# Optimization experiments

Measured on AMD Instinct MI355X. Metric: run time of the kernel, lower is better.

Reference implementation:

```python
import jax, jax.numpy as jnp
import numpy as np

N = 8192
E = 524288
IN_DIM = 128
HID = 256
OUT_DIM = 128
N_LAYERS = 3
N_HEADS = 4
HEAD_DIM = HID // N_HEADS


def setup_inputs() -> dict:
    key = jax.random.key(0)
    ks = jax.random.split(key, 12)
    s = 0.05
    return {
        "x": jax.random.normal(ks[0], (N, IN_DIM), dtype=jnp.float32),
        "edge_index": jax.random.randint(ks[1], (2, E), 0, N, dtype=jnp.int64),
        "W_in": jax.random.normal(ks[2], (HID, IN_DIM), dtype=jnp.float32) * s,
        "b_in": jnp.zeros((HID,), dtype=jnp.float32),
        "plasticity": jnp.ones((N_LAYERS,), dtype=jnp.float32),
        "synaptic": jnp.ones((N_LAYERS,), dtype=jnp.float32),
        "in_proj_w": jax.random.normal(ks[3], (3 * HID, HID), dtype=jnp.float32) * s,
        "in_proj_b": jnp.zeros((3 * HID,), dtype=jnp.float32),
        "out_proj_w": jax.random.normal(ks[4], (HID, HID), dtype=jnp.float32) * s,
        "out_proj_b": jnp.zeros((HID,), dtype=jnp.float32),
        "W_out": jax.random.normal(ks[5], (OUT_DIM, HID), dtype=jnp.float32) * s,
        "b_out": jnp.zeros((OUT_DIM,), dtype=jnp.float32),
    }


def _forward(x, edge_index, W_in, b_in, plasticity, synaptic,
             in_proj_w, in_proj_b, out_proj_w, out_proj_b, W_out, b_out):
    src, dst = edge_index[0], edge_index[1]  # x_j = x[src], aggregate at dst (source_to_target)
    x = x @ W_in.T + b_in  # [N, HID]
    for i in range(N_LAYERS):
        x = x * jax.nn.sigmoid(plasticity[i])
        # message: x_j * sigmoid(synaptic) (scalar edge weight); aggr='add'
        agg = jax.ops.segment_sum(x[src], dst, num_segments=N)  # gather-scatter-add
        x = jax.nn.leaky_relu(agg * jax.nn.sigmoid(synaptic[i]), negative_slope=0.01)
    # MultiheadAttention over all N nodes (seq_len=N, batch=1)
    qkv = x @ in_proj_w.T + in_proj_b  # [N, 3*HID]
    q, k, v = jnp.split(qkv, 3, axis=-1)
    q = q.reshape(N, N_HEADS, HEAD_DIM).transpose(1, 0, 2)  # [h, n, d]
    k = k.reshape(N, N_HEADS, HEAD_DIM).transpose(1, 0, 2)
    v = v.reshape(N, N_HEADS, HEAD_DIM).transpose(1, 0, 2)
    scores = jnp.einsum("hnd,hmd->hnm", q, k) / np.sqrt(HEAD_DIM).astype(np.float32)
    attn = jax.nn.softmax(scores, axis=-1)
    o = jnp.einsum("hnm,hmd->hnd", attn, v)  # [h, n, d]
    o = o.transpose(1, 0, 2).reshape(N, HID)
    x = o @ out_proj_w.T + out_proj_b
    return x @ W_out.T + b_out  # [N, OUT_DIM]


def reference(x, edge_index, W_in, b_in, plasticity, synaptic,
              in_proj_w, in_proj_b, out_proj_w, out_proj_b, W_out, b_out):
    return _forward(x, edge_index, W_in, b_in, plasticity, synaptic,
                    in_proj_w, in_proj_b, out_proj_w, out_proj_b, W_out, b_out)
```

## Files before the change

### kernel.cpp

```cpp
#include <hip/hip_runtime.h>
#include <hip/hip_bf16.h>
#include <float.h>

#define N_NODES 8192
#define NEDGE   524288
#define IND     128
#define HID     256
#define OUTD    128
#define NHEAD   4
#define HD      64

typedef short short8 __attribute__((ext_vector_type(8)));
typedef short short4v __attribute__((ext_vector_type(4)));
typedef float f32x4  __attribute__((ext_vector_type(4)));
typedef float f32x16 __attribute__((ext_vector_type(16)));
typedef unsigned int u32x4 __attribute__((ext_vector_type(4)));

__device__ __forceinline__ float sigmoidf_(float x) { return 1.0f / (1.0f + expf(-x)); }

__device__ __forceinline__ unsigned short f2bf(float f) {
    __hip_bfloat16 b = __float2bfloat16(f);
    return __builtin_bit_cast(unsigned short, b);
}
__device__ __forceinline__ float bf2f(unsigned short u) {
    __hip_bfloat16 b = __builtin_bit_cast(__hip_bfloat16, u);
    return __bfloat162float(b);
}
__device__ __forceinline__ void split3(float x, unsigned short& a, unsigned short& b, unsigned short& c) {
    a = f2bf(x); float r = x - bf2f(a);
    b = f2bf(r); r = r - bf2f(b);
    c = f2bf(r);
}
__device__ __forceinline__ void split2(float x, unsigned short& a, unsigned short& b) {
    a = f2bf(x); float r = x - bf2f(a);
    b = f2bf(r);
}
__device__ __forceinline__ unsigned int cvtpk(float lo, float hi) {
    unsigned int r;
    asm("v_cvt_pk_bf16_f32 %0, %1, %2" : "=v"(r) : "v"(lo), "v"(hi));
    return r;
}
__device__ __forceinline__ void plswap(unsigned int& a, unsigned int& b) {
    asm volatile("v_permlane32_swap_b32 %0, %1" : "+v"(a), "+v"(b));
}
__device__ __forceinline__ void gll16(const void* g, void* l) {
    __builtin_amdgcn_global_load_lds(
        (const __attribute__((address_space(1))) void*)g,
        (__attribute__((address_space(3))) void*)l, 16, 0, 0);
}
__device__ __forceinline__ f32x16 mfma32(short8 a, short8 b, f32x16 c) {
    return __builtin_amdgcn_mfma_f32_32x32x16_bf16(a, b, c, 0, 0, 0);
}

__global__ void hist_kernel(const int* __restrict__ ei, int* __restrict__ deg)
{
    int e = blockIdx.x * blockDim.x + threadIdx.x;
    if (e < NEDGE) atomicAdd(&deg[ei[NEDGE + e]], 1);
}

__global__ __launch_bounds__(1024) void scan_kernel(
    const int* __restrict__ deg, int* __restrict__ row_ptr, int* __restrict__ cursor)
{
    __shared__ int sh[1024];
    const int t = threadIdx.x;
    int v[8]; int s = 0;
    #pragma unroll
    for (int i = 0; i < 8; ++i) { v[i] = deg[t * 8 + i]; s += v[i]; }
    sh[t] = s; __syncthreads();
    for (int off = 1; off < 1024; off <<= 1) {
        int add = (t >= off) ? sh[t - off] : 0;
        __syncthreads();
        sh[t] += add;
        __syncthreads();
    }
    int base = sh[t] - s;
    #pragma unroll
    for (int i = 0; i < 8; ++i) {
        row_ptr[t * 8 + i] = base;
        cursor[t * 8 + i]  = base;
        base += v[i];
    }
    if (t == 1023) row_ptr[N_NODES] = base;
}

__global__ void scatter_kernel(const int* __restrict__ ei, int* __restrict__ cursor,
                               int* __restrict__ esrc)
{
    int e = blockIdx.x * blockDim.x + threadIdx.x;
    if (e < NEDGE) {
        int d = ei[NEDGE + e];
        int p = atomicAdd(&cursor[d], 1);
        esrc[p] = ei[e];
    }
}

__global__ __launch_bounds__(256) void split_w_kernel(
    const float* __restrict__ w, unsigned short* __restrict__ Wc, int elems)
{
    const int i = (blockIdx.x * 256 + threadIdx.x) * 8;
    if (i >= elems) return;
    float4 a = *(const float4*)(w + i);
    float4 b = *(const float4*)(w + i + 4);
    float v[8] = {a.x, a.y, a.z, a.w, b.x, b.y, b.z, b.w};
    short8 c0, c1, c2;
    #pragma unroll
    for (int j = 0; j < 8; ++j) {
        unsigned short p, q, r;
        split3(v[j], p, q, r);
        c0[j] = (short)p; c1[j] = (short)q; c2[j] = (short)r;
    }
    *(short8*)(Wc + i) = c0;
    *(short8*)(Wc + elems + i) = c1;
    *(short8*)(Wc + 2 * elems + i) = c2;
}

__global__ __launch_bounds__(256) void aggregate_sliced_kernel(
    const float* __restrict__ hin, float* __restrict__ hout,
    const int* __restrict__ row_ptr, const int* __restrict__ esrc,
    const float* __restrict__ plas, const float* __restrict__ syn, int layer)
{
    const int b = blockIdx.x;
    const int xs = b & 7, g = b >> 3;
    const int slice = xs & 3, halfn = xs >> 2;
    const int t = threadIdx.x;
    const int dst = halfn * 4096 + g * 4 + (t >> 6);
    const int col = slice * 64 + (t & 63);
    const int st = row_ptr[dst], en = row_ptr[dst + 1];
    float a0 = 0.f, a1 = 0.f, a2 = 0.f, a3 = 0.f;
    int e = st;
    for (; e + 4 <= en; e += 4) {
        int s0 = esrc[e], s1 = esrc[e + 1], s2 = esrc[e + 2], s3 = esrc[e + 3];
        a0 += hin[(size_t)s0 * HID + col];
        a1 += hin[(size_t)s1 * HID + col];
        a2 += hin[(size_t)s2 * HID + col];
        a3 += hin[(size_t)s3 * HID + col];
    }
    float acc = (a0 + a1) + (a2 + a3);
    for (; e < en; ++e) acc += hin[(size_t)esrc[e] * HID + col];
    const float scale = sigmoidf_(plas[layer]) * sigmoidf_(syn[layer]);
    float x = acc * scale;
    hout[(size_t)dst * HID + col] = (x > 0.f) ? x : 0.01f * x;
}

__global__ __launch_bounds__(256) void aggregate_sliced_split_kernel(
    const float* __restrict__ hin,
    unsigned short* __restrict__ H0, unsigned short* __restrict__ H1,
    unsigned short* __restrict__ H2,
    const int* __restrict__ row_ptr, const int* __restrict__ esrc,
    const float* __restrict__ plas, const float* __restrict__ syn, int layer)
{
    const int b = blockIdx.x;
    const int xs = b & 7, g = b >> 3;
    const int slice = xs & 3, halfn = xs >> 2;
    const int t = threadIdx.x;
    const int dst = halfn * 4096 + g * 4 + (t >> 6);
    const int col = slice * 64 + (t & 63);
    const int st = row_ptr[dst], en = row_ptr[dst + 1];
    float a0 = 0.f, a1 = 0.f, a2 = 0.f, a3 = 0.f;
    int e = st;
    for (; e + 4 <= en; e += 4) {
        int s0 = esrc[e], s1 = esrc[e + 1], s2 = esrc[e + 2], s3 = esrc[e + 3];
        a0 += hin[(size_t)s0 * HID + col];
        a1 += hin[(size_t)s1 * HID + col];
        a2 += hin[(size_t)s2 * HID + col];
        a3 += hin[(size_t)s3 * HID + col];
    }
    float acc = (a0 + a1) + (a2 + a3);
    for (; e < en; ++e) acc += hin[(size_t)esrc[e] * HID + col];
    const float scale = sigmoidf_(plas[layer]) * sigmoidf_(syn[layer]);
    float x = acc * scale;
    x = (x > 0.f) ? x : 0.01f * x;
    unsigned short p, q, r;
    split3(x, p, q, r);
    H0[(size_t)dst * HID + col] = p;
    H1[(size_t)dst * HID + col] = q;
    H2[(size_t)dst * HID + col] = r;
}

template<int NT, int NA, bool SOUT>
__global__ __launch_bounds__(256) void mfma_gemm_kernel(
    const unsigned short* __restrict__ A0, const unsigned short* __restrict__ A1,
    const unsigned short* __restrict__ A2,
    const unsigned short* __restrict__ Wc, const float* __restrict__ bias,
    float* __restrict__ Cf, unsigned short* __restrict__ C0, unsigned short* __restrict__ C1,
    int M, int Nn, int K)
{
    const int t = threadIdx.x;
    const int wv = t >> 6, lane = t & 63;
    const int l31 = lane & 31, l5 = lane >> 5;
    const int wm = wv & 1, wn = wv >> 1;
    const int m0 = blockIdx.x * 64 + wm * 32;
    const int n0 = blockIdx.y * 64 + wn * 32;
    const int mrow = m0 + l31;
    const int nrow = n0 + l31;
    const size_t NK = (size_t)Nn * K;

    f32x16 o;
    #pragma unroll
    for (int r = 0; r < 16; ++r) o[r] = 0.f;

    for (int k = 0; k < K; k += 16) {
        const int kk = k + l5 * 8;
        short8 af[NA];
        af[0] = *(const short8*)(A0 + (size_t)mrow * K + kk);
        af[1] = *(const short8*)(A1 + (size_t)mrow * K + kk);
        if (NA > 2) af[2] = *(const short8*)(A2 + (size_t)mrow * K + kk);
        const unsigned short* wp = Wc + (size_t)nrow * K + kk;
        short8 w0 = *(const short8*)(wp);
        short8 w1 = *(const short8*)(wp + NK);
        if (NT == 6) {
            short8 w2 = *(const short8*)(wp + 2 * NK);
            o = mfma32(w0, af[2], o);
            o = mfma32(w1, af[1], o);
            o = mfma32(w2, af[0], o);
            o = mfma32(w0, af[1], o);
            o = mfma32(w1, af[0], o);
            o = mfma32(w0, af[0], o);
        } else {
            o = mfma32(w0, af[1], o);
            o = mfma32(w1, af[0], o);
            o = mfma32(w0, af[0], o);
        }
    }

    #pragma unroll
    for (int g = 0; g < 4; ++g) {
        const int nb = n0 + g * 8 + l5 * 4;
        const float4 b4 = *(const float4*)(bias + nb);
        float v0 = o[4 * g + 0] + b4.x;
        float v1 = o[4 * g + 1] + b4.y;
        float v2 = o[4 * g + 2] + b4.z;
        float v3 = o[4 * g + 3] + b4.w;
        if (!SOUT) {
            float4 st = {v0, v1, v2, v3};
            *(float4*)(Cf + (size_t)mrow * Nn + nb) = st;
        } else {
            unsigned short h0, h1, p0, p1, q0, q1, r0, r1;
            split2(v0, h0, h1); split2(v1, p0, p1);
            split2(v2, q0, q1); split2(v3, r0, r1);
            short4v s0 = {(short)h0, (short)p0, (short)q0, (short)r0};
            short4v s1 = {(short)h1, (short)p1, (short)q1, (short)r1};
            *(short4v*)(C0 + (size_t)mrow * Nn + nb) = s0;
            *(short4v*)(C1 + (size_t)mrow * Nn + nb) = s1;
        }
    }
}

__global__ __launch_bounds__(256) void split_kernel(
    const float* __restrict__ qkv,
    unsigned short* __restrict__ Kc0, unsigned short* __restrict__ Kc1,
    unsigned short* __restrict__ Kc2, unsigned short* __restrict__ Vt0)
{
    __shared__ unsigned short vts[64 * 80];
    const int h  = blockIdx.y;
    const int n0 = blockIdx.x * 64;
    const int t  = threadIdx.x;
    const int r  = t >> 2;
    const int n  = n0 + r;
    const int dc = (t & 3) * 16;

    {
        const float* kp = qkv + (size_t)n * 768 + 256 + h * 64 + dc;
        float kv[16];
        #pragma unroll
        for (int i = 0; i < 16; i += 4) {
            float4 f = *(const float4*)(kp + i);
            kv[i] = f.x; kv[i+1] = f.y; kv[i+2] = f.z; kv[i+3] = f.w;
        }
        #pragma unroll
        for (int half = 0; half < 2; ++half) {
            short8 c0, c1, c2;
            #pragma unroll
            for (int j = 0; j < 8; ++j) {
                unsigned short a, b, c;
                split3(kv[half * 8 + j], a, b, c);
                c0[j] = (short)a; c1[j] = (short)b; c2[j] = (short)c;
            }
            const int pos = ((dc >> 3) + half) ^ (n & 7);
            const size_t base = ((size_t)(h * 8192 + n)) * 64 + pos * 8;
            *(short8*)(Kc0 + base) = c0;
            *(short8*)(Kc1 + base) = c1;
            *(short8*)(Kc2 + base) = c2;
        }
    }
    {
        const float* vp = qkv + (size_t)n * 768 + 512 + h * 64 + dc;
        #pragma unroll
        for (int i = 0; i < 16; i += 4) {
            float4 f = *(const float4*)(vp + i);
            float vv[4] = {f.x, f.y, f.z, f.w};
            #pragma unroll
            for (int k2 = 0; k2 < 4; ++k2)
                vts[(dc + i + k2) * 80 + r] = f2bf(vv[k2]);
        }
    }
    __syncthreads();
    #pragma unroll
    for (int i = 0; i < 2; ++i) {
        const int q = t * 2 + i;
        const int d = q >> 3, nc = q & 7;
        const int g = nc >> 2, c = nc & 3;
        short8 vv = *(const short8*)(&vts[d * 80 + nc * 8]);
        const size_t dst = ((size_t)(h * 64 + d)) * 8192 + n0 + g * 32 + ((c ^ (d & 3)) * 8);
        *(short8*)(Vt0 + dst) = vv;
    }
}

__global__ __launch_bounds__(256, 4) void attn_mfma_kernel(
    const float* __restrict__ qkv,
    const unsigned short* __restrict__ Kc0, const unsigned short* __restrict__ Kc1,
    const unsigned short* __restrict__ Kc2, const unsigned short* __restrict__ Vt0,
    unsigned short* __restrict__ Op16, float* __restrict__ Ml)
{
    __shared__ __align__(16) char smem[32768];
    const int h    = blockIdx.y;
    const int quar = blockIdx.z;
    const int n0   = blockIdx.x * 128;
    const int t    = threadIdx.x;
    const int wv   = t >> 6;
    const int lane = t & 63;
    const int l31  = lane & 31, l5 = lane >> 5;
    const int qbase = n0 + wv * 32;

    const float QSC = 0.125f * 1.4426950408889634f;
    short8 qf[3][4];
    #pragma unroll
    for (int ks = 0; ks < 4; ++ks) {
        const float* qp = qkv + (size_t)(qbase + l31) * 768 + h * 64 + ks * 16 + l5 * 8;
        float4 qa = *(const float4*)qp, qb4 = *(const float4*)(qp + 4);
        float qv[8] = {qa.x, qa.y, qa.z, qa.w, qb4.x, qb4.y, qb4.z, qb4.w};
        #pragma unroll
        for (int j = 0; j < 8; ++j) {
            unsigned short a, b, c;
            split3(qv[j] * QSC, a, b, c);
            qf[0][ks][j] = (short)a;
            qf[1][ks][j] = (short)b;
            qf[2][ks][j] = (short)c;
        }
    }

    int koff[4], voff[2][2];
    #pragma unroll
    for (int ks = 0; ks < 4; ++ks)
        koff[ks] = l31 * 128 + (((ks * 2 + l5) ^ (l31 & 7)) * 16);
    #pragma unroll
    for (int ks = 0; ks < 2; ++ks)
        #pragma unroll
        for (int db = 0; db < 2; ++db) {
            const int d = db * 32 + l31;
            voff[ks][db] = 12288 + d * 64 + (((ks * 2 + l5) ^ (d & 3)) * 16);
        }

    const char* sgb[4];
    int ldso[4];
    #pragma unroll
    for (int i = 0; i < 4; ++i) {
        const int s = wv * 4 + i;
        if (s < 12) {
            const int c = s >> 2, rb = s & 3;
            const unsigned short* base = (c == 0) ? Kc0 : (c == 1) ? Kc1 : Kc2;
            const int row = rb * 8 + (lane >> 3);
            sgb[i] = (const char*)(base + ((size_t)(h * 8192 + quar * 2048 + row)) * 64 + (lane & 7) * 8);
            ldso[i] = c * 4096 + rb * 1024;
        } else {
            const int v = s - 12;
            const int d = v * 16 + (lane >> 2);
            sgb[i] = (const char*)(Vt0 + ((size_t)(h * 64 + d)) * 8192 + quar * 2048 + (lane & 3) * 8);
            ldso[i] = 12288 + v * 1024;
        }
    }
    const size_t ktstride = (wv < 3) ? 4096 : 64;

    auto STAGE = [&](int kt, int bb) {
        #pragma unroll
        for (int i = 0; i < 4; ++i)
            gll16(sgb[i] + (size_t)kt * ktstride, &smem[bb * 16384 + ldso[i]]);
    };

    f32x16 o[2];
    #pragma unroll
    for (int db = 0; db < 2; ++db)
        #pragma unroll
        for (int r = 0; r < 16; ++r) o[db][r] = 0.f;
    float mr = -FLT_MAX, ls = 0.f;

    STAGE(0, 0);
    __syncthreads();

    for (int kt = 0; kt < 64; ++kt) {
        const int bb = kt & 1;
        if (kt < 63) STAGE(kt + 1, bb ^ 1);
        const char* buf = &smem[bb * 16384];

        f32x16 s;
        #pragma unroll
        for (int r = 0; r < 16; ++r) s[r] = 0.f;

        __builtin_amdgcn_s_setprio(1);
        #pragma unroll
        for (int ks = 0; ks < 4; ++ks) {
            const int off = koff[ks];
            short8 k0 = *(const short8*)(buf + off);
            short8 k1 = *(const short8*)(buf + 4096 + off);
            short8 k2 = *(const short8*)(buf + 8192 + off);
            s = mfma32(k0, qf[2][ks], s);
            s = mfma32(k1, qf[1][ks], s);
            s = mfma32(k2, qf[0][ks], s);
            s = mfma32(k0, qf[1][ks], s);
            s = mfma32(k1, qf[0][ks], s);
            s = mfma32(k0, qf[0][ks], s);
        }
        __builtin_amdgcn_s_setprio(0);

        float mx = s[0];
        #pragma unroll
        for (int r = 1; r < 16; ++r) mx = fmaxf(mx, s[r]);
        mx = fmaxf(mx, __shfl_xor(mx, 32));
        if (__any(mx > mr + 12.0f)) {
            const float mn = fmaxf(mr, mx);
            const float alpha = exp2f(mr - mn);
            mr = mn;
            ls *= alpha;
            o[0] *= alpha;
            o[1] *= alpha;
        }
        float ps = 0.f;
        #pragma unroll
        for (int r = 0; r < 16; ++r) {
            float p = exp2f(s[r] - mr);
            s[r] = p;
            ps += p;
        }
        ps += __shfl_xor(ps, 32);
        ls += ps;

        short8 pb[2];
        #pragma unroll
        for (int ks = 0; ks < 2; ++ks) {
            const int rb = ks * 8;
            unsigned int A0 = cvtpk(s[rb + 0], s[rb + 1]);
            unsigned int A1 = cvtpk(s[rb + 2], s[rb + 3]);
            unsigned int B0 = cvtpk(s[rb + 4], s[rb + 5]);
            unsigned int B1 = cvtpk(s[rb + 6], s[rb + 7]);
            plswap(A0, B0);
            plswap(A1, B1);
            u32x4 pw; pw[0] = A0; pw[1] = A1; pw[2] = B0; pw[3] = B1;
            pb[ks] = __builtin_bit_cast(short8, pw);
        }

        __builtin_amdgcn_s_setprio(1);
        #pragma unroll
        for (int ks = 0; ks < 2; ++ks) {
            #pragma unroll
            for (int db = 0; db < 2; ++db) {
                short8 v = *(const short8*)(buf + voff[ks][db]);
                o[db] = mfma32(v, pb[ks], o[db]);
            }
        }
        __builtin_amdgcn_s_setprio(0);

        __syncthreads();
    }

    {
        const int q = qbase + l31;
        unsigned short* opq = Op16 + ((size_t)((quar * 4 + h) * 8192 + q)) * 64;
        #pragma unroll
        for (int db = 0; db < 2; ++db) {
            #pragma unroll
            for (int tq = 0; tq < 4; ++tq) {
                const int d0 = db * 32 + tq * 8 + l5 * 4;
                unsigned int w0 = cvtpk(o[db][4 * tq + 0], o[db][4 * tq + 1]);
                unsigned int w1 = cvtpk(o[db][4 * tq + 2], o[db][4 * tq + 3]);
                uint2 st = {w0, w1};
                *(uint2*)(opq + d0) = st;
            }
        }
        if (l5 == 0) {
            Ml[((size_t)(quar * 4 + h) * 2 + 0) * 8192 + q] = mr;
            Ml[((size_t)(quar * 4 + h) * 2 + 1) * 8192 + q] = ls;
        }
    }
}

__global__ __launch_bounds__(256) void combine_kernel(
    const unsigned short* __restrict__ Op16, const float* __restrict__ Ml,
    unsigned short* __restrict__ aO0, unsigned short* __restrict__ aO1)
{
    const int idx = blockIdx.x * 256 + threadIdx.x;
    const int c = idx & 3;
    const int q = (idx >> 2) & 8191;
    const int h = idx >> 15;
    float m[4], l[4];
    float mg = -FLT_MAX;
    #pragma unroll
    for (int s = 0; s < 4; ++s) {
        m[s] = Ml[((size_t)(s * 4 + h) * 2 + 0) * 8192 + q];
        l[s] = Ml[((size_t)(s * 4 + h) * 2 + 1) * 8192 + q];
        mg = fmaxf(mg, m[s]);
    }
    float w[4], denom = 0.f;
    #pragma unroll
    for (int s = 0; s < 4; ++s) {
        w[s] = exp2f(m[s] - mg);
        denom += l[s] * w[s];
    }
    const float inv = 1.f / denom;
    float acc[16] = {};
    #pragma unroll
    for (int s = 0; s < 4; ++s) {
        const unsigned short* p = Op16 + ((size_t)(s * 4 + h) * 8192 + q) * 64 + c * 16;
        short8 v0 = *(const short8*)(p);
        short8 v1 = *(const short8*)(p + 8);
        #pragma unroll
        for (int i = 0; i < 8; ++i) {
            acc[i]     += w[s] * bf2f((unsigned short)v0[i]);
            acc[i + 8] += w[s] * bf2f((unsigned short)v1[i]);
        }
    }
    unsigned short* d0 = aO0 + (size_t)q * 256 + h * 64 + c * 16;
    unsigned short* d1 = aO1 + (size_t)q * 256 + h * 64 + c * 16;
    short8 o0, o1;
    #pragma unroll
    for (int i = 0; i < 8; ++i) {
        unsigned short a, b;
        split2(acc[i] * inv, a, b);
        o0[i] = (short)a; o1[i] = (short)b;
    }
    *(short8*)(d0) = o0;
    *(short8*)(d1) = o1;
    #pragma unroll
    for (int i = 0; i < 8; ++i) {
        unsigned short a, b;
        split2(acc[i + 8] * inv, a, b);
        o0[i] = (short)a; o1[i] = (short)b;
    }
    *(short8*)(d0 + 8) = o0;
    *(short8*)(d1 + 8) = o1;
}

extern "C" void kernel_launch(void* const* d_in, const int* in_sizes, int n_in,
                              void* d_out, int out_size, void* d_ws, size_t ws_size,
                              hipStream_t stream)
{
    const float* x     = (const float*)d_in[0];
    const int*   ei    = (const int*)  d_in[1];
    const float* W_in  = (const float*)d_in[2];
    const float* b_in  = (const float*)d_in[3];
    const float* plas  = (const float*)d_in[4];
    const float* syn   = (const float*)d_in[5];
    const float* inpw  = (const float*)d_in[6];
    const float* inpb  = (const float*)d_in[7];
    const float* outpw = (const float*)d_in[8];
    const float* outpb = (const float*)d_in[9];
    const float* Wout  = (const float*)d_in[10];
    const float* bout  = (const float*)d_in[11];
    float* out = (float*)d_out;

    char* ws = (char*)d_ws;
    float* h    = (float*)(ws + 0);
    float* h2   = (float*)(ws + (8u  << 20));
    float* qkv  = (float*)(ws + (16u << 20));
    unsigned short* xc0  = (unsigned short*)(ws + (16u << 20));
    unsigned short* xc1  = (unsigned short*)(ws + (18u << 20));
    unsigned short* xc2  = (unsigned short*)(ws + (20u << 20));
    unsigned short* h2c0 = (unsigned short*)(ws + (8u  << 20));
    unsigned short* h2c1 = (unsigned short*)(ws + (12u << 20));
    unsigned short* h2c2 = (unsigned short*)(ws + (40u << 20));
    unsigned short* Wic  = (unsigned short*)(ws + (44u << 20));
    unsigned short* ipc  = (unsigned short*)(ws + (45u << 20));
    unsigned short* opc  = (unsigned short*)(ws + (16u << 20));
    unsigned short* woc  = (unsigned short*)(ws + (17u << 20));
    unsigned short* Kc0  = (unsigned short*)(ws + 0);
    unsigned short* Kc1  = (unsigned short*)(ws + (4u  << 20));
    unsigned short* Kc2  = (unsigned short*)(ws + (8u  << 20));
    unsigned short* Vt0  = (unsigned short*)(ws + (12u << 20));
    unsigned short* Op16 = (unsigned short*)(ws + (40u << 20));
    unsigned short* aOc0 = (unsigned short*)(ws + 0);
    unsigned short* aOc1 = (unsigned short*)(ws + (4u  << 20));
    unsigned short* tmpc0 = (unsigned short*)(ws + (8u  << 20));
    unsigned short* tmpc1 = (unsigned short*)(ws + (12u << 20));
    int*   rowp = (int*)(ws + (56u << 20));
    int*   curs = (int*)(ws + (56u << 20) + 40960);
    int*   esrc = (int*)(ws + (56u << 20) + 81920);
    float* Ml   = (float*)(ws + (56u << 20) + 81920);

    hipMemsetAsync(curs, 0, N_NODES * sizeof(int), stream);
    hist_kernel<<<NEDGE / 256, 256, 0, stream>>>(ei, curs);
    scan_kernel<<<1, 1024, 0, stream>>>(curs, rowp, curs);
    scatter_kernel<<<NEDGE / 256, 256, 0, stream>>>(ei, curs, esrc);

    split_w_kernel<<<(HID * IND) / 2048, 256, 0, stream>>>(W_in, Wic, HID * IND);
    split_w_kernel<<<(768 * HID) / 2048, 256, 0, stream>>>(inpw, ipc, 768 * HID);
    split_w_kernel<<<(N_NODES * IND) / 2048, 256, 0, stream>>>(x, xc0, N_NODES * IND);

    mfma_gemm_kernel<6, 3, false><<<dim3(N_NODES / 64, HID / 64), 256, 0, stream>>>(
        xc0, xc0 + N_NODES * IND, xc0 + 2 * N_NODES * IND, Wic, b_in,
        h, nullptr, nullptr, N_NODES, HID, IND);

    aggregate_sliced_kernel<<<N_NODES, 256, 0, stream>>>(h,  h2, rowp, esrc, plas, syn, 0);
    aggregate_sliced_kernel<<<N_NODES, 256, 0, stream>>>(h2, h,  rowp, esrc, plas, syn, 1);
    aggregate_sliced_split_kernel<<<N_NODES, 256, 0, stream>>>(h, h2c0, h2c1, h2c2,
                                                               rowp, esrc, plas, syn, 2);

    mfma_gemm_kernel<6, 3, false><<<dim3(N_NODES / 64, 768 / 64), 256, 0, stream>>>(
        h2c0, h2c1, h2c2, ipc, inpb, qkv, nullptr, nullptr, N_NODES, 768, HID);

    split_kernel<<<dim3(N_NODES / 64, NHEAD), 256, 0, stream>>>(
        qkv, Kc0, Kc1, Kc2, Vt0);

    attn_mfma_kernel<<<dim3(N_NODES / 128, NHEAD, 4), 256, 0, stream>>>(
        qkv, Kc0, Kc1, Kc2, Vt0, Op16, Ml);

    combine_kernel<<<512, 256, 0, stream>>>(Op16, Ml, aOc0, aOc1);

    split_w_kernel<<<(HID * HID) / 2048, 256, 0, stream>>>(outpw, opc, HID * HID);
    split_w_kernel<<<(OUTD * HID) / 2048, 256, 0, stream>>>(Wout, woc, OUTD * HID);

    mfma_gemm_kernel<3, 2, true><<<dim3(N_NODES / 64, HID / 64), 256, 0, stream>>>(
        aOc0, aOc1, nullptr, opc, outpb, nullptr, tmpc0, tmpc1, N_NODES, HID, HID);
    mfma_gemm_kernel<3, 2, false><<<dim3(N_NODES / 64, OUTD / 64), 256, 0, stream>>>(
        tmpc0, tmpc1, nullptr, woc, bout, out, nullptr, nullptr, N_NODES, OUTD, HID);
}
```

Measured before the change: 613.1 us.

## Vectorize aggregation, triple-buffer attention with QK lookahead, halve key splits

The graph aggregation kernels are merged into one template in which each thread gathers float4 rows for four columns, so 2048 blocks cover 16 destination nodes each instead of 8192 blocks with scalar loads. The attention kernel now uses a three-buffer LDS ring with stages two tiles ahead and raw s_barrier/waitcnt. It computes QK for the next tile while doing softmax and PV on the current one. The key dimension is split into 2 parts instead of 4, which means fewer blocks (occupancy bound 2), a larger shared allocation and a simpler combine step.

```diff
diff --git a/kernel.cpp b/kernel.cpp
--- a/kernel.cpp
+++ b/kernel.cpp
@@ -114,67 +114,65 @@
     *(short8*)(Wc + 2 * elems + i) = c2;
 }
 
-__global__ __launch_bounds__(256) void aggregate_sliced_kernel(
+template<int SPLIT>
+__global__ __launch_bounds__(256) void aggregate4_kernel(
     const float* __restrict__ hin, float* __restrict__ hout,
-    const int* __restrict__ row_ptr, const int* __restrict__ esrc,
-    const float* __restrict__ plas, const float* __restrict__ syn, int layer)
-{
-    const int b = blockIdx.x;
-    const int xs = b & 7, g = b >> 3;
-    const int slice = xs & 3, halfn = xs >> 2;
-    const int t = threadIdx.x;
-    const int dst = halfn * 4096 + g * 4 + (t >> 6);
-    const int col = slice * 64 + (t & 63);
-    const int st = row_ptr[dst], en = row_ptr[dst + 1];
-    float a0 = 0.f, a1 = 0.f, a2 = 0.f, a3 = 0.f;
-    int e = st;
-    for (; e + 4 <= en; e += 4) {
-        int s0 = esrc[e], s1 = esrc[e + 1], s2 = esrc[e + 2], s3 = esrc[e + 3];
-        a0 += hin[(size_t)s0 * HID + col];
-        a1 += hin[(size_t)s1 * HID + col];
-        a2 += hin[(size_t)s2 * HID + col];
-        a3 += hin[(size_t)s3 * HID + col];
-    }
-    float acc = (a0 + a1) + (a2 + a3);
-    for (; e < en; ++e) acc += hin[(size_t)esrc[e] * HID + col];
-    const float scale = sigmoidf_(plas[layer]) * sigmoidf_(syn[layer]);
-    float x = acc * scale;
-    hout[(size_t)dst * HID + col] = (x > 0.f) ? x : 0.01f * x;
-}
-
-__global__ __launch_bounds__(256) void aggregate_sliced_split_kernel(
-    const float* __restrict__ hin,
     unsigned short* __restrict__ H0, unsigned short* __restrict__ H1,
     unsigned short* __restrict__ H2,
     const int* __restrict__ row_ptr, const int* __restrict__ esrc,
     const float* __restrict__ plas, const float* __restrict__ syn, int layer)
 {
     const int b = blockIdx.x;
-    const int xs = b & 7, g = b >> 3;
-    const int slice = xs & 3, halfn = xs >> 2;
+    const int slice = b & 3, gb = b >> 2;
     const int t = threadIdx.x;
-    const int dst = halfn * 4096 + g * 4 + (t >> 6);
-    const int col = slice * 64 + (t & 63);
+    const int g = t >> 4;
+    const int c4 = (t & 15) * 4;
+    const int dst = gb * 16 + g;
+    const int col = slice * 64 + c4;
     const int st = row_ptr[dst], en = row_ptr[dst + 1];
-    float a0 = 0.f, a1 = 0.f, a2 = 0.f, a3 = 0.f;
+
+    float a0x=0,a0y=0,a0z=0,a0w=0, a1x=0,a1y=0,a1z=0,a1w=0;
+    float a2x=0,a2y=0,a2z=0,a2w=0, a3x=0,a3y=0,a3z=0,a3w=0;
     int e = st;
     for (; e + 4 <= en; e += 4) {
         int s0 = esrc[e], s1 = esrc[e + 1], s2 = esrc[e + 2], s3 = esrc[e + 3];
-        a0 += hin[(size_t)s0 * HID + col];
-        a1 += hin[(size_t)s1 * HID + col];
-        a2 += hin[(size_t)s2 * HID + col];
-        a3 += hin[(size_t)s3 * HID + col];
-    }
-    float acc = (a0 + a1) + (a2 + a3);
-    for (; e < en; ++e) acc += hin[(size_t)esrc[e] * HID + col];
+        float4 v0 = *(const float4*)(hin + (size_t)s0 * HID + col);
+        float4 v1 = *(const float4*)(hin + (size_t)s1 * HID + col);
+        float4 v2 = *(const float4*)(hin + (size_t)s2 * HID + col);
+        float4 v3 = *(const float4*)(hin + (size_t)s3 * HID + col);
+        a0x += v0.x; a0y += v0.y; a0z += v0.z; a0w += v0.w;
+        a1x += v1.x; a1y += v1.y; a1z += v1.z; a1w += v1.w;
+        a2x += v2.x; a2y += v2.y; a2z += v2.z; a2w += v2.w;
+        a3x += v3.x; a3y += v3.y; a3z += v3.z; a3w += v3.w;
+    }
+    float rx = (a0x + a1x) + (a2x + a3x);
+    float ry = (a0y + a1y) + (a2y + a3y);
+    float rz = (a0z + a1z) + (a2z + a3z);
+    float rw = (a0w + a1w) + (a2w + a3w);
+    for (; e < en; ++e) {
+        float4 v = *(const float4*)(hin + (size_t)esrc[e] * HID + col);
+        rx += v.x; ry += v.y; rz += v.z; rw += v.w;
+    }
     const float scale = sigmoidf_(plas[layer]) * sigmoidf_(syn[layer]);
-    float x = acc * scale;
-    x = (x > 0.f) ? x : 0.01f * x;
-    unsigned short p, q, r;
-    split3(x, p, q, r);
-    H0[(size_t)dst * HID + col] = p;
-    H1[(size_t)dst * HID + col] = q;
-    H2[(size_t)dst * HID + col] = r;
+    float o4[4] = {rx * scale, ry * scale, rz * scale, rw * scale};
+    #pragma unroll
+    for (int i = 0; i < 4; ++i) o4[i] = (o4[i] > 0.f) ? o4[i] : 0.01f * o4[i];
+
+    if (SPLIT == 0) {
+        float4 stv = {o4[0], o4[1], o4[2], o4[3]};
+        *(float4*)(hout + (size_t)dst * HID + col) = stv;
+    } else {
+        short4v h0, h1, h2;
+        #pragma unroll
+        for (int i = 0; i < 4; ++i) {
+            unsigned short p, q, r;
+            split3(o4[i], p, q, r);
+            h0[i] = (short)p; h1[i] = (short)q; h2[i] = (short)r;
+        }
+        *(short4v*)(H0 + (size_t)dst * HID + col) = h0;
+        *(short4v*)(H1 + (size_t)dst * HID + col) = h1;
+        *(short4v*)(H2 + (size_t)dst * HID + col) = h2;
+    }
 }
 
 template<int NT, int NA, bool SOUT>
@@ -232,8 +230,8 @@
         float v2 = o[4 * g + 2] + b4.z;
         float v3 = o[4 * g + 3] + b4.w;
         if (!SOUT) {
-            float4 st = {v0, v1, v2, v3};
-            *(float4*)(Cf + (size_t)mrow * Nn + nb) = st;
+            float4 stv = {v0, v1, v2, v3};
+            *(float4*)(Cf + (size_t)mrow * Nn + nb) = stv;
         } else {
             unsigned short h0, h1, p0, p1, q0, q1, r0, r1;
             split2(v0, h0, h1); split2(v1, p0, p1);
@@ -306,15 +304,15 @@
     }
 }
 
-__global__ __launch_bounds__(256, 4) void attn_mfma_kernel(
+__global__ __launch_bounds__(256, 2) void attn_pipe_kernel(
     const float* __restrict__ qkv,
     const unsigned short* __restrict__ Kc0, const unsigned short* __restrict__ Kc1,
     const unsigned short* __restrict__ Kc2, const unsigned short* __restrict__ Vt0,
     unsigned short* __restrict__ Op16, float* __restrict__ Ml)
 {
-    __shared__ __align__(16) char smem[32768];
+    __shared__ __align__(16) char smem[49152];
     const int h    = blockIdx.y;
-    const int quar = blockIdx.z;
+    const int half = blockIdx.z;
     const int n0   = blockIdx.x * 128;
     const int t    = threadIdx.x;
     const int wv   = t >> 6;
@@ -360,21 +358,21 @@
             const int c = s >> 2, rb = s & 3;
             const unsigned short* base = (c == 0) ? Kc0 : (c == 1) ? Kc1 : Kc2;
             const int row = rb * 8 + (lane >> 3);
-            sgb[i] = (const char*)(base + ((size_t)(h * 8192 + quar * 2048 + row)) * 64 + (lane & 7) * 8);
+            sgb[i] = (const char*)(base + ((size_t)(h * 8192 + half * 4096 + row)) * 64 + (lane & 7) * 8);
             ldso[i] = c * 4096 + rb * 1024;
         } else {
             const int v = s - 12;
             const int d = v * 16 + (lane >> 2);
-            sgb[i] = (const char*)(Vt0 + ((size_t)(h * 64 + d)) * 8192 + quar * 2048 + (lane & 3) * 8);
+            sgb[i] = (const char*)(Vt0 + ((size_t)(h * 64 + d)) * 8192 + half * 4096 + (lane & 3) * 8);
             ldso[i] = 12288 + v * 1024;
         }
     }
     const size_t ktstride = (wv < 3) ? 4096 : 64;
 
-    auto STAGE = [&](int kt, int bb) {
+    auto STAGE = [&](int kt, int bo) {
         #pragma unroll
         for (int i = 0; i < 4; ++i)
-            gll16(sgb[i] + (size_t)kt * ktstride, &smem[bb * 16384 + ldso[i]]);
+            gll16(sgb[i] + (size_t)kt * ktstride, &smem[bo + ldso[i]]);
     };
 
     f32x16 o[2];
@@ -384,87 +382,113 @@
         for (int r = 0; r < 16; ++r) o[db][r] = 0.f;
     float mr = -FLT_MAX, ls = 0.f;
 
-    STAGE(0, 0);
-    __syncthreads();
-
-    for (int kt = 0; kt < 64; ++kt) {
-        const int bb = kt & 1;
-        if (kt < 63) STAGE(kt + 1, bb ^ 1);
-        const char* buf = &smem[bb * 16384];
-
-        f32x16 s;
-        #pragma unroll
-        for (int r = 0; r < 16; ++r) s[r] = 0.f;
-
+    auto QK = [&](const char* buf, f32x16& sreg) {
+        #pragma unroll
+        for (int r = 0; r < 16; ++r) sreg[r] = 0.f;
         __builtin_amdgcn_s_setprio(1);
         #pragma unroll
         for (int ks = 0; ks < 4; ++ks) {
-            const int off = koff[ks];
-            short8 k0 = *(const short8*)(buf + off);
-            short8 k1 = *(const short8*)(buf + 4096 + off);
-            short8 k2 = *(const short8*)(buf + 8192 + off);
-            s = mfma32(k0, qf[2][ks], s);
-            s = mfma32(k1, qf[1][ks], s);
-            s = mfma32(k2, qf[0][ks], s);
-            s = mfma32(k0, qf[1][ks], s);
-            s = mfma32(k1, qf[0][ks], s);
-            s = mfma32(k0, qf[0][ks], s);
+            short8 k0 = *(const short8*)(buf + koff[ks]);
+            short8 k1 = *(const short8*)(buf + 4096 + koff[ks]);
+            short8 k2 = *(const short8*)(buf + 8192 + koff[ks]);
+            sreg = mfma32(k0, qf[2][ks], sreg);
+            sreg = mfma32(k1, qf[1][ks], sreg);
+            sreg = mfma32(k2, qf[0][ks], sreg);
+            sreg = mfma32(k0, qf[1][ks], sreg);
+            sreg = mfma32(k1, qf[0][ks], sreg);
+            sreg = mfma32(k0, qf[0][ks], sreg);
         }
         __builtin_amdgcn_s_setprio(0);
-
-        float mx = s[0];
-        #pragma unroll
-        for (int r = 1; r < 16; ++r) mx = fmaxf(mx, s[r]);
+    };
+
+    int cb = 0, nb = 16384, fb = 32768;
+
+    auto ITER = [&](int kt, f32x16& scur, f32x16& snxt) {
+        const bool more = (kt + 2) < 128;
+        if (more) {
+            STAGE(kt + 2, fb);
+            asm volatile("s_waitcnt vmcnt(4)" ::: "memory");
+        } else {
+            asm volatile("s_waitcnt vmcnt(0)" ::: "memory");
+        }
+        __builtin_amdgcn_s_barrier();
+        __builtin_amdgcn_sched_barrier(0);
+
+        if (kt + 1 < 128) QK(&smem[nb], snxt);
+
+        float mx = scur[0];
+        #pragma unroll
+        for (int r = 1; r < 16; ++r) mx = fmaxf(mx, scur[r]);
         mx = fmaxf(mx, __shfl_xor(mx, 32));
         if (__any(mx > mr + 12.0f)) {
             const float mn = fmaxf(mr, mx);
-            const float alpha = exp2f(mr - mn);
-            mr = mn;
-            ls *= alpha;
-            o[0] *= alpha;
-            o[1] *= alpha;
+            const float al = exp2f(mr - mn);
+            mr = mn; ls *= al;
+            o[0] *= al; o[1] *= al;
         }
         float ps = 0.f;
         #pragma unroll
         for (int r = 0; r < 16; ++r) {
-            float p = exp2f(s[r] - mr);
-            s[r] = p;
+            float p = exp2f(scur[r] - mr);
+            scur[r] = p;
             ps += p;
         }
         ps += __shfl_xor(ps, 32);
         ls += ps;
 
-        short8 pb[2];
-        #pragma unroll
-        for (int ks = 0; ks < 2; ++ks) {
-            const int rb = ks * 8;
-            unsigned int A0 = cvtpk(s[rb + 0], s[rb + 1]);
-            unsigned int A1 = cvtpk(s[rb + 2], s[rb + 3]);
-            unsigned int B0 = cvtpk(s[rb + 4], s[rb + 5]);
-            unsigned int B1 = cvtpk(s[rb + 6], s[rb + 7]);
-            plswap(A0, B0);
-            plswap(A1, B1);
+        short8 pb0, pb1;
+        {
+            unsigned int A0 = cvtpk(scur[0], scur[1]);
+            unsigned int A1 = cvtpk(scur[2], scur[3]);
+            unsigned int B0 = cvtpk(scur[4], scur[5]);
+            unsigned int B1 = cvtpk(scur[6], scur[7]);
+            plswap(A0, B0); plswap(A1, B1);
             u32x4 pw; pw[0] = A0; pw[1] = A1; pw[2] = B0; pw[3] = B1;
-            pb[ks] = __builtin_bit_cast(short8, pw);
+            pb0 = __builtin_bit_cast(short8, pw);
+            unsigned int C0_ = cvtpk(scur[8],  scur[9]);
+            unsigned int C1_ = cvtpk(scur[10], scur[11]);
+            unsigned int D0 = cvtpk(scur[12], scur[13]);
+            unsigned int D1 = cvtpk(scur[14], scur[15]);
+            plswap(C0_, D0); plswap(C1_, D1);
+            u32x4 pw2; pw2[0] = C0_; pw2[1] = C1_; pw2[2] = D0; pw2[3] = D1;
+            pb1 = __builtin_bit_cast(short8, pw2);
         }
 
         __builtin_amdgcn_s_setprio(1);
-        #pragma unroll
-        for (int ks = 0; ks < 2; ++ks) {
-            #pragma unroll
-            for (int db = 0; db < 2; ++db) {
-                short8 v = *(const short8*)(buf + voff[ks][db]);
-                o[db] = mfma32(v, pb[ks], o[db]);
-            }
+        {
+            const char* bufc = &smem[cb];
+            short8 v00 = *(const short8*)(bufc + voff[0][0]);
+            short8 v01 = *(const short8*)(bufc + voff[0][1]);
+            o[0] = mfma32(v00, pb0, o[0]);
+            o[1] = mfma32(v01, pb0, o[1]);
+            short8 v10 = *(const short8*)(bufc + voff[1][0]);
+            short8 v11 = *(const short8*)(bufc + voff[1][1]);
+            o[0] = mfma32(v10, pb1, o[0]);
+            o[1] = mfma32(v11, pb1, o[1]);
         }
         __builtin_amdgcn_s_setprio(0);
 
-        __syncthreads();
+        __builtin_amdgcn_sched_barrier(0);
+        __builtin_amdgcn_s_barrier();
+        int tmp = cb; cb = nb; nb = fb; fb = tmp;
+    };
+
+    STAGE(0, 0);
+    STAGE(1, 16384);
+    asm volatile("s_waitcnt vmcnt(4)" ::: "memory");
+    __builtin_amdgcn_s_barrier();
+    __builtin_amdgcn_sched_barrier(0);
+    f32x16 sA, sB;
+    QK(&smem[0], sA);
+
+    for (int kt = 0; kt < 128; kt += 2) {
+        ITER(kt,     sA, sB);
+        ITER(kt + 1, sB, sA);
     }
 
     {
         const int q = qbase + l31;
-        unsigned short* opq = Op16 + ((size_t)((quar * 4 + h) * 8192 + q)) * 64;
+        unsigned short* opq = Op16 + ((size_t)((half * 4 + h) * 8192 + q)) * 64;
         #pragma unroll
         for (int db = 0; db < 2; ++db) {
             #pragma unroll
@@ -472,13 +496,13 @@
                 const int d0 = db * 32 + tq * 8 + l5 * 4;
                 unsigned int w0 = cvtpk(o[db][4 * tq + 0], o[db][4 * tq + 1]);
                 unsigned int w1 = cvtpk(o[db][4 * tq + 2], o[db][4 * tq + 3]);
-                uint2 st = {w0, w1};
-                *(uint2*)(opq + d0) = st;
+                uint2 stv = {w0, w1};
+                *(uint2*)(opq + d0) = stv;
             }
         }
         if (l5 == 0) {
-            Ml[((size_t)(quar * 4 + h) * 2 + 0) * 8192 + q] = mr;
-            Ml[((size_t)(quar * 4 + h) * 2 + 1) * 8192 + q] = ls;
+            Ml[((size_t)(half * 4 + h) * 2 + 0) * 8192 + q] = mr;
+            Ml[((size_t)(half * 4 + h) * 2 + 1) * 8192 + q] = ls;
         }
     }
 }
@@ -491,24 +515,20 @@
     const int c = idx & 3;
     const int q = (idx >> 2) & 8191;
     const int h = idx >> 15;
-    float m[4], l[4];
-    float mg = -FLT_MAX;
-    #pragma unroll
-    for (int s = 0; s < 4; ++s) {
+    float m[2], l[2];
+    #pragma unroll
+    for (int s = 0; s < 2; ++s) {
         m[s] = Ml[((size_t)(s * 4 + h) * 2 + 0) * 8192 + q];
         l[s] = Ml[((size_t)(s * 4 + h) * 2 + 1) * 8192 + q];
-        mg = fmaxf(mg, m[s]);
-    }
-    float w[4], denom = 0.f;
-    #pragma unroll
-    for (int s = 0; s < 4; ++s) {
-        w[s] = exp2f(m[s] - mg);
-        denom += l[s] * w[s];
-    }
-    const float inv = 1.f / denom;
+    }
+    const float mg = fmaxf(m[0], m[1]);
+    float w[2];
+    w[0] = exp2f(m[0] - mg);
+    w[1] = exp2f(m[1] - mg);
+    const float inv = 1.f / (l[0] * w[0] + l[1] * w[1]);
     float acc[16] = {};
     #pragma unroll
-    for (int s = 0; s < 4; ++s) {
+    for (int s = 0; s < 2; ++s) {
         const unsigned short* p = Op16 + ((size_t)(s * 4 + h) * 8192 + q) * 64 + c * 16;
         short8 v0 = *(const short8*)(p);
         short8 v1 = *(const short8*)(p + 8);
@@ -562,8 +582,6 @@
     float* h2   = (float*)(ws + (8u  << 20));
     float* qkv  = (float*)(ws + (16u << 20));
     unsigned short* xc0  = (unsigned short*)(ws + (16u << 20));
-    unsigned short* xc1  = (unsigned short*)(ws + (18u << 20));
-    unsigned short* xc2  = (unsigned short*)(ws + (20u << 20));
     unsigned short* h2c0 = (unsigned short*)(ws + (8u  << 20));
     unsigned short* h2c1 = (unsigned short*)(ws + (12u << 20));
     unsigned short* h2c2 = (unsigned short*)(ws + (40u << 20));
@@ -598,10 +616,12 @@
         xc0, xc0 + N_NODES * IND, xc0 + 2 * N_NODES * IND, Wic, b_in,
         h, nullptr, nullptr, N_NODES, HID, IND);
 
-    aggregate_sliced_kernel<<<N_NODES, 256, 0, stream>>>(h,  h2, rowp, esrc, plas, syn, 0);
-    aggregate_sliced_kernel<<<N_NODES, 256, 0, stream>>>(h2, h,  rowp, esrc, plas, syn, 1);
-    aggregate_sliced_split_kernel<<<N_NODES, 256, 0, stream>>>(h, h2c0, h2c1, h2c2,
-                                                               rowp, esrc, plas, syn, 2);
+    aggregate4_kernel<0><<<2048, 256, 0, stream>>>(h,  h2, nullptr, nullptr, nullptr,
+                                                   rowp, esrc, plas, syn, 0);
+    aggregate4_kernel<0><<<2048, 256, 0, stream>>>(h2, h,  nullptr, nullptr, nullptr,
+                                                   rowp, esrc, plas, syn, 1);
+    aggregate4_kernel<1><<<2048, 256, 0, stream>>>(h, nullptr, h2c0, h2c1, h2c2,
+                                                   rowp, esrc, plas, syn, 2);
 
     mfma_gemm_kernel<6, 3, false><<<dim3(N_NODES / 64, 768 / 64), 256, 0, stream>>>(
         h2c0, h2c1, h2c2, ipc, inpb, qkv, nullptr, nullptr, N_NODES, 768, HID);
@@ -609,7 +629,7 @@
     split_kernel<<<dim3(N_NODES / 64, NHEAD), 256, 0, stream>>>(
         qkv, Kc0, Kc1, Kc2, Vt0);
 
-    attn_mfma_kernel<<<dim3(N_NODES / 128, NHEAD, 4), 256, 0, stream>>>(
+    attn_pipe_kernel<<<dim3(N_NODES / 128, NHEAD, 2), 256, 0, stream>>>(
         qkv, Kc0, Kc1, Kc2, Vt0, Op16, Ml);
 
     combine_kernel<<<512, 256, 0, stream>>>(Op16, Ml, aOc0, aOc1);
```

Measured after the change: 569.6 us. 7.1% less time.
